# Performance work log

Hardware: AMD Instinct MI355X
Metric: run time of the kernel (lower is better)

Reference implementation:

```python
import jax, jax.numpy as jnp
from jax import lax
import numpy as np
import math

B, T, D, H, DFF, L = 64, 351, 512, 8, 1024, 3
DK = D // H
SQRT_DIM = math.sqrt(D)


def setup_inputs() -> dict:
    key = jax.random.key(0)
    ks = jax.random.split(key, 32)
    s = 0.02
    n = lambda k, shape, sc=s: jax.random.normal(k, shape, jnp.float32) * sc
    inp = {
        'x': jax.random.normal(ks[0], (B, T, D), jnp.float32),
        'mask': jax.random.normal(ks[1], (B, T, D), jnp.float32),  # float stream: used as pos_embedding inside attention
        'pos_emb': n(ks[2], (L, T, D)),           # Encoder.pos_embedding_{1,2,3}
        'Wq': n(ks[3], (L, D, D)), 'bq': jnp.zeros((L, D), jnp.float32),
        'Wk': n(ks[4], (L, D, D)), 'bk': jnp.zeros((L, D), jnp.float32),
        'Wv': n(ks[5], (L, D, D)), 'bv': jnp.zeros((L, D), jnp.float32),
        'Wp': n(ks[6], (L, D, D)),                 # pos_proj, no bias
        'u_bias': n(ks[7], (L, H, DK)), 'v_bias': n(ks[8], (L, H, DK)),
        'Wo': n(ks[9], (L, D, D)), 'bo': jnp.zeros((L, D), jnp.float32),
        'ln1_a': jnp.ones((L, D), jnp.float32), 'ln1_b': jnp.zeros((L, D), jnp.float32),
        'ln2_a': jnp.ones((L, D), jnp.float32), 'ln2_b': jnp.zeros((L, D), jnp.float32),
        'W1': n(ks[10], (L, DFF, D)), 'b1': jnp.zeros((L, DFF), jnp.float32),   # conv1d k=1
        'W2': n(ks[11], (L, D, DFF, 3)), 'b2': jnp.zeros((L, D), jnp.float32),  # conv1d k=3 pad=1
        'fn_a': jnp.ones((D,), jnp.float32), 'fn_b': jnp.zeros((D,), jnp.float32),
    }
    return inp


def layernorm(x, a, b, eps=1e-6):
    # torch: a*(x-mean)/(std+eps)+b with unbiased std (Bessel, n-1)
    mean = x.mean(-1, keepdims=True)
    xc = x - mean
    std = jnp.sqrt((xc * xc).sum(-1, keepdims=True) / (x.shape[-1] - 1))
    return a * xc / (std + eps) + b


def rel_shift(ps):
    # Transformer-XL relative shift via pad+reshape
    b, h, t1, t2 = ps.shape
    p = jnp.pad(ps, ((0, 0), (0, 0), (0, 0), (1, 0)))
    p = p.reshape(b, h, t2 + 1, t1)
    return p[:, :, 1:].reshape(b, h, t1, t2)


def attention(xn, pe, Wq, bq, Wk, bk, Wv, bv, Wp, u, v, Wo, bo):
    b, t, _ = xn.shape
    q = (xn @ Wq.T + bq).reshape(b, t, H, DK)
    k = (xn @ Wk.T + bk).reshape(b, t, H, DK)
    val = (xn @ Wv.T + bv).reshape(b, t, H, DK)
    p = (pe @ Wp.T).reshape(b, t, H, DK)
    content = jnp.einsum('bqhd,bkhd->bhqk', q + u, k)
    pos = rel_shift(jnp.einsum('bqhd,bkhd->bhqk', q + v, p))
    attn = jax.nn.softmax((content + pos) / SQRT_DIM, axis=-1)  # mask=None path; dropout inactive (eval)
    ctx = jnp.einsum('bhqk,bkhd->bqhd', attn, val).reshape(b, t, D)
    return ctx @ Wo.T + bo


def reference(x, mask, pos_emb, Wq, bq, Wk, bk, Wv, bv, Wp, u_bias, v_bias, Wo, bo,
              ln1_a, ln1_b, ln2_a, ln2_b, W1, b1, W2, b2, fn_a, fn_b):
    for i in range(L):
        x = x + pos_emb[i][None]
        # sublayer 0: pre-LN relative MHA with residual (stride_num[i]==1)
        xn = layernorm(x, ln1_a[i], ln1_b[i])
        x = x + attention(xn, mask, Wq[i], bq[i], Wk[i], bk[i], Wv[i], bv[i],
                          Wp[i], u_bias[i], v_bias[i], Wo[i], bo[i])
        # sublayer 1: pre-LN conv FFN (k=1 conv -> ReLU -> k=3 conv, pad 1, stride 1)
        xn = layernorm(x, ln2_a[i], ln2_b[i])
        h = jax.nn.relu(jnp.einsum('btd,fd->btf', xn, W1[i]) + b1[i])
        y = lax.conv_general_dilated(h.transpose(0, 2, 1), W2[i], (1,), [(1, 1)],
                                     dimension_numbers=('NCH', 'OIH', 'NCH'))
        x = x + (y + b2[i][None, :, None]).transpose(0, 2, 1)
    return layernorm(x, fn_a, fn_b)
```

## Files before the change

### kernel.cpp

```cpp
#include <hip/hip_runtime.h>
#include <hip/hip_bf16.h>

typedef __hip_bfloat16 bf16;
typedef __attribute__((ext_vector_type(8))) short short8;
typedef __attribute__((ext_vector_type(4))) float f32x4;

constexpr int BB  = 64;
constexpr int TT  = 351;
constexpr int DD  = 512;
constexpr int HH  = 8;
constexpr int DK  = 64;
constexpr int FF  = 1024;
constexpr int LL  = 3;
constexpr int MT  = BB * TT;
constexpr int TD  = TT * DD;

constexpr int QT  = 16;
constexpr int NQT = (TT + QT - 1) / QT;

constexpr size_t LW      = 3407872;
constexpr size_t OFF_QKV = 0;
constexpr size_t OFF_P   = 786432;
constexpr size_t OFF_O   = 1048576;
constexpr size_t OFF_W1  = 1310720;
constexpr size_t OFF_W2  = 1835008;

__device__ __forceinline__ float us2f(unsigned short u) {
    union { unsigned int i; float f; } c; c.i = ((unsigned int)u) << 16; return c.f;
}
__device__ __forceinline__ float bf2f(bf16 h) { return __bfloat162float(h); }
__device__ __forceinline__ bf16  f2bf(float f) { return __float2bfloat16(f); }
__device__ __forceinline__ float ldin(const void* p, size_t i, bool f32) {
    return f32 ? ((const float*)p)[i] : bf2f(((const bf16*)p)[i]);
}
__device__ __forceinline__ unsigned short f2us(float f) {
    bf16 h = f2bf(f); return *reinterpret_cast<unsigned short*>(&h);
}

__global__ void detect_kernel(const unsigned short* ln1a, int* flag) {
    if (threadIdx.x == 0 && blockIdx.x == 0)
        *flag = (ln1a[0] == 0) ? 1 : 0;
}

__global__ __launch_bounds__(256) void cvt_kernel(
    const void* __restrict__ src, size_t S, size_t slstride,
    bf16* __restrict__ dst, size_t doff, int nl, int mode,
    const int* __restrict__ dflag)
{
    const bool f32 = (*dflag != 0);
    size_t i = (size_t)blockIdx.x * 256 + threadIdx.x;
    size_t total = (size_t)nl * S;
    if (i >= total) return;
    size_t l = i / S, e = i - l * S;
    size_t se;
    if (mode == 1) {
        size_t j = e >> 19;
        size_t nf = e & ((1u << 19) - 1);
        size_t n = nf >> 10, f = nf & 1023;
        se = n * 3072 + f * 3 + j;
    } else se = e;
    dst[doff + l * LW + e] = f2bf(ldin(src, l * slstride + se, f32));
}

__global__ __launch_bounds__(256) void addpos_kernel(
    const void* __restrict__ xin, const void* __restrict__ pos, size_t posoff,
    float* __restrict__ xf, int init, const int* __restrict__ dflag)
{
    const bool f32 = (*dflag != 0);
    int i = blockIdx.x * 256 + threadIdx.x;
    if (i >= MT * DD) return;
    int td = i % TD;
    float p = ldin(pos, posoff + td, f32);
    if (init) xf[i] = ldin(xin, i, f32) + p;
    else      xf[i] += p;
}

__global__ __launch_bounds__(256) void ln_kernel(
    const float* __restrict__ xf, const void* __restrict__ ga, size_t gaoff,
    const void* __restrict__ gb, size_t gboff,
    void* __restrict__ out, int final_o, const int* __restrict__ dflag)
{
    const bool f32 = (*dflag != 0);
    __shared__ float red[256];
    const int row = blockIdx.x;
    const int tid = threadIdx.x;
    const float* xr = xf + (size_t)row * DD;
    float x0 = xr[tid], x1 = xr[tid + 256];

    red[tid] = x0 + x1;
    __syncthreads();
    for (int o = 128; o > 0; o >>= 1) {
        if (tid < o) red[tid] += red[tid + o];
        __syncthreads();
    }
    float mean = red[0] * (1.0f / 512.0f);
    __syncthreads();
    float c0 = x0 - mean, c1 = x1 - mean;
    red[tid] = c0 * c0 + c1 * c1;
    __syncthreads();
    for (int o = 128; o > 0; o >>= 1) {
        if (tid < o) red[tid] += red[tid + o];
        __syncthreads();
    }
    float stdv = sqrtf(red[0] * (1.0f / 511.0f));
    float inv = 1.0f / (stdv + 1e-6f);
    float v0 = ldin(ga, gaoff + tid,       f32) * c0 * inv + ldin(gb, gboff + tid,       f32);
    float v1 = ldin(ga, gaoff + tid + 256, f32) * c1 * inv + ldin(gb, gboff + tid + 256, f32);
    if (final_o && f32) {
        float* orow = (float*)out + (size_t)row * DD;
        orow[tid] = v0; orow[tid + 256] = v1;
    } else {
        bf16* orow = (bf16*)out + (size_t)row * DD;
        orow[tid] = f2bf(v0); orow[tid + 256] = f2bf(v1);
    }
}

__device__ __forceinline__ void xcd_remap(int& bx, int& by) {
    int gx = gridDim.x, gy = gridDim.y;
    int nb = gx * gy;
    int d  = by * gx + bx;
    if ((nb & 7) == 0) {
        int q = nb >> 3;
        d = (d & 7) * q + (d >> 3);
        bx = d % gx;
        by = d / gx;
    }
}

__global__ __launch_bounds__(256) void mgemm_kernel(
    const void* __restrict__ A, size_t aoff, int a_ext,
    const bf16* __restrict__ W,
    const void* __restrict__ b0, const void* __restrict__ b1p,
    const void* __restrict__ b2p, size_t boff,
    void* __restrict__ outp, int M, int N, int K, int mode, int chN,
    const int* __restrict__ dflag)
{
    const bool f32 = (*dflag != 0);
    const bool a32 = a_ext && f32;
    __shared__ unsigned short As[128][40];
    __shared__ unsigned short Bs[128][40];
    const int tid = threadIdx.x;
    int bx = blockIdx.x, by = blockIdx.y;
    xcd_remap(bx, by);
    const int n0 = bx * 128, m0 = by * 128;

    const int lane = tid & 63, wv = tid >> 6;
    const int wm = wv >> 1, wn = wv & 1;
    const int q = lane >> 4, lm = lane & 15;

    f32x4 acc[4][4] = {};

    for (int k0 = 0; k0 < K; k0 += 32) {
        #pragma unroll
        for (int part = 0; part < 2; ++part) {
            int idx = part * 256 + tid;
            int row = idx >> 2;
            int seg = (idx & 3) * 8;
            int grow = m0 + row; if (grow >= M) grow = M - 1;
            if (a32) {
                const float* ap = (const float*)A + aoff + (size_t)grow * K + k0 + seg;
                union { unsigned short us[8]; int4 v; } t;
                #pragma unroll
                for (int e = 0; e < 8; ++e) t.us[e] = f2us(ap[e]);
                *(int4*)&As[row][seg] = t.v;
            } else {
                *(int4*)&As[row][seg] =
                    *(const int4*)((const bf16*)A + aoff + (size_t)grow * K + k0 + seg);
            }
            *(int4*)&Bs[row][seg] =
                *(const int4*)(W + (size_t)(n0 + row) * K + k0 + seg);
        }
        __syncthreads();
        short8 af[4], bfv[4];
        #pragma unroll
        for (int i = 0; i < 4; ++i) af[i]  = *(const short8*)&As[wm * 64 + i * 16 + lm][q * 8];
        #pragma unroll
        for (int j = 0; j < 4; ++j) bfv[j] = *(const short8*)&Bs[wn * 64 + j * 16 + lm][q * 8];
        #pragma unroll
        for (int i = 0; i < 4; ++i)
            #pragma unroll
            for (int j = 0; j < 4; ++j)
                acc[i][j] = __builtin_amdgcn_mfma_f32_16x16x32_bf16(af[i], bfv[j], acc[i][j], 0, 0, 0);
        __syncthreads();
    }

    #pragma unroll
    for (int i = 0; i < 4; ++i) {
        #pragma unroll
        for (int j = 0; j < 4; ++j) {
            #pragma unroll
            for (int r = 0; r < 4; ++r) {
                int m = m0 + wm * 64 + i * 16 + q * 4 + r;
                if (m >= M) continue;
                int n = n0 + wn * 64 + j * 16 + lm;
                float c = acc[i][j][r];
                if (mode == 0) {
                    int which = n >> 9;
                    int nn = n & 511;
                    const void* bp = which == 0 ? b0 : (which == 1 ? b1p : b2p);
                    if (bp) c += ldin(bp, boff + nn, f32);
                    int b = m / TT, t = m - b * TT;
                    int h = nn >> 6, dk = nn & 63;
                    ((bf16*)outp)[(size_t)which * chN +
                                  ((((size_t)b * HH + h) * TT + t) * DK) + dk] = f2bf(c);
                } else if (mode == 1) {
                    if (b0) c += ldin(b0, boff + n, f32);
                    ((bf16*)outp)[(size_t)m * N + n] = f2bf(fmaxf(c, 0.0f));
                } else {
                    if (b0) c += ldin(b0, boff + n, f32);
                    ((float*)outp)[(size_t)m * DD + n] += c;
                }
            }
        }
    }
}

__global__ __launch_bounds__(256) void mconv_kernel(
    const bf16* __restrict__ Hb, const bf16* __restrict__ Wc,
    const void* __restrict__ bias, size_t boff,
    float* __restrict__ xf, int M, const int* __restrict__ dflag)
{
    const bool f32 = (*dflag != 0);
    __shared__ unsigned short As[128][40];
    __shared__ unsigned short Bs[128][40];
    const int tid = threadIdx.x;
    int bx = blockIdx.x, by = blockIdx.y;
    xcd_remap(bx, by);
    const int n0 = bx * 128, m0 = by * 128;

    const int lane = tid & 63, wv = tid >> 6;
    const int wm = wv >> 1, wn = wv & 1;
    const int q = lane >> 4, lm = lane & 15;

    int rowP[2], segP[2], mloadP[2], trowP[2];
    bool inrP[2];
    #pragma unroll
    for (int part = 0; part < 2; ++part) {
        int idx = part * 256 + tid;
        rowP[part] = idx >> 2;
        segP[part] = (idx & 3) * 8;
        int mrow = m0 + rowP[part];
        inrP[part] = mrow < M;
        int mload = inrP[part] ? mrow : (M - 1);
        mloadP[part] = mload;
        trowP[part] = mload % TT;
    }

    f32x4 acc[4][4] = {};

    for (int j = 0; j < 3; ++j) {
        for (int k0 = 0; k0 < FF; k0 += 32) {
            #pragma unroll
            for (int part = 0; part < 2; ++part) {
                int row = rowP[part], seg = segP[part];
                int ts = trowP[part] + j - 1;
                bool valid = inrP[part] && ts >= 0 && ts < TT;
                if (valid) {
                    *(int4*)&As[row][seg] =
                        *(const int4*)(Hb + (size_t)(mloadP[part] + j - 1) * FF + k0 + seg);
                } else {
                    int4 z = {0, 0, 0, 0};
                    *(int4*)&As[row][seg] = z;
                }
                *(int4*)&Bs[row][seg] =
                    *(const int4*)(Wc + (size_t)j * 524288 + (size_t)(n0 + row) * FF + k0 + seg);
            }
            __syncthreads();
            short8 af[4], bfv[4];
            #pragma unroll
            for (int i = 0; i < 4; ++i) af[i]  = *(const short8*)&As[wm * 64 + i * 16 + lm][q * 8];
            #pragma unroll
            for (int jj = 0; jj < 4; ++jj) bfv[jj] = *(const short8*)&Bs[wn * 64 + jj * 16 + lm][q * 8];
            #pragma unroll
            for (int i = 0; i < 4; ++i)
                #pragma unroll
                for (int jj = 0; jj < 4; ++jj)
                    acc[i][jj] = __builtin_amdgcn_mfma_f32_16x16x32_bf16(af[i], bfv[jj], acc[i][jj], 0, 0, 0);
            __syncthreads();
        }
    }

    #pragma unroll
    for (int i = 0; i < 4; ++i) {
        #pragma unroll
        for (int jj = 0; jj < 4; ++jj) {
            #pragma unroll
            for (int r = 0; r < 4; ++r) {
                int m = m0 + wm * 64 + i * 16 + q * 4 + r;
                if (m >= M) continue;
                int n = n0 + wn * 64 + jj * 16 + lm;
                xf[(size_t)m * DD + n] += acc[i][jj][r] + ldin(bias, boff + n, f32);
            }
        }
    }
}

__global__ __launch_bounds__(256, 4) void attn_kernel(
    const bf16* __restrict__ Q, const bf16* __restrict__ Kb,
    const bf16* __restrict__ V, const bf16* __restrict__ P,
    const void* __restrict__ ubias, const void* __restrict__ vbias, size_t uvoff,
    bf16* __restrict__ ctx, const int* __restrict__ dflag)
{
    const bool f32 = (*dflag != 0);
    const int d  = blockIdx.x + NQT * (blockIdx.y + HH * blockIdx.z);
    const int rr = d % (8 * NQT);
    const int g  = (d / (8 * NQT)) * 8 + (rr & 7);
    const int t  = rr >> 3;
    const int b  = g >> 3;
    const int h  = g & 7;
    const int q0 = t * QT;

    const int tid  = threadIdx.x;
    const int lane = tid & 63;
    const int wv   = tid >> 6;
    const int lm   = lane & 15;
    const int q8   = lane >> 4;

    __shared__ __align__(16) float S[QT][354];
    __shared__ __align__(16) unsigned short Abf[QT][356];
    __shared__ __align__(16) unsigned short qu[QT][72];
    __shared__ __align__(16) unsigned short qv[QT + 2][72];

    const size_t base = (((size_t)b * HH + h) * TT) * DK;
    const float scale = 0.04419417382415922f;

    for (int i = tid; i < (QT + 1) * 64; i += 256) {
        int q = i >> 6, dd = i & 63;
        int qrow = q0 + q;
        float qq = (qrow < TT) ? bf2f(Q[base + (size_t)qrow * DK + dd]) : 0.0f;
        float vb = ldin(vbias, uvoff + h * DK + dd, f32);
        qv[q][dd] = f2us((qq + vb) * scale);
        if (q < QT) {
            float ub = ldin(ubias, uvoff + h * DK + dd, f32);
            qu[q][dd] = f2us((qq + ub) * scale);
        }
    }
    __syncthreads();

    short8 kv0[6], kv1[6], pv0[6], pv1[6];
    #pragma unroll
    for (int it = 0; it < 6; ++it) {
        int jt = wv + it * 4;
        int kr = jt * 16 + lm; if (kr > TT - 1) kr = TT - 1;
        const short8* kp = (const short8*)(Kb + base + (size_t)kr * DK + q8 * 8);
        const short8* pp = (const short8*)(P  + base + (size_t)kr * DK + q8 * 8);
        kv0[it] = kp[0]; kv1[it] = kp[4];
        pv0[it] = pp[0]; pv1[it] = pp[4];
    }

    {
        short8 afa = *(const short8*)&qu[lm][q8 * 8];
        short8 afb = *(const short8*)&qu[lm][32 + q8 * 8];
        #pragma unroll
        for (int it = 0; it < 6; ++it) {
            int jt = wv + it * 4;
            if (jt >= NQT) break;
            f32x4 a0 = {};
            a0 = __builtin_amdgcn_mfma_f32_16x16x32_bf16(afa, kv0[it], a0, 0, 0, 0);
            a0 = __builtin_amdgcn_mfma_f32_16x16x32_bf16(afb, kv1[it], a0, 0, 0, 0);
            int col = jt * 16 + lm;
            #pragma unroll
            for (int r = 0; r < 4; ++r)
                S[q8 * 4 + r][col] = a0[r];
        }
    }
    __syncthreads();

    {
        short8 af0a = *(const short8*)&qv[lm][q8 * 8];
        short8 af0b = *(const short8*)&qv[lm][32 + q8 * 8];
        short8 af1a = {}, af1b = {};
        if (lm == 0) {
            af1a = *(const short8*)&qv[QT][q8 * 8];
            af1b = *(const short8*)&qv[QT][32 + q8 * 8];
        }
        #pragma unroll
        for (int it = 0; it < 6; ++it) {
            int jt = wv + it * 4;
            if (jt >= NQT) break;
            f32x4 ac0 = {}, ac1 = {};
            ac0 = __builtin_amdgcn_mfma_f32_16x16x32_bf16(af0a, pv0[it], ac0, 0, 0, 0);
            ac0 = __builtin_amdgcn_mfma_f32_16x16x32_bf16(af0b, pv1[it], ac0, 0, 0, 0);
            ac1 = __builtin_amdgcn_mfma_f32_16x16x32_bf16(af1a, pv0[it], ac1, 0, 0, 0);
            ac1 = __builtin_amdgcn_mfma_f32_16x16x32_bf16(af1b, pv1[it], ac1, 0, 0, 0);
            int j = jt * 16 + lm;
            if (j < TT) {
                #pragma unroll
                for (int i = 0; i < 2; ++i) {
                    #pragma unroll
                    for (int r = 0; r < 4; ++r) {
                        int rl = i * 16 + q8 * 4 + r;
                        int rg = q0 + rl;
                        float v = (i == 0) ? ac0[r] : ac1[r];
                        int cb  = (j + rg < TT - 1) ? 1 : 0;
                        int row = rl - cb;
                        int col = j + rg - (TT - 1) + cb * TT;
                        if (row >= 0 && row < QT) S[row][col] += v;
                    }
                }
            }
        }
    }
    __syncthreads();

    const unsigned short* vcol = (const unsigned short*)(V + base) + (wv * 16 + lm);
    short8 bvv[11];
    #pragma unroll
    for (int ks = 0; ks < 11; ++ks) {
        #pragma unroll
        for (int e = 0; e < 8; ++e) {
            int k = ks * 32 + q8 * 8 + e;
            bvv[ks][e] = (k < TT) ? (short)vcol[(size_t)k * DK] : (short)0;
        }
    }

    {
        const int row = tid >> 4, k0 = tid & 15;
        const float* Sr = S[row];
        float sv[22];
        #pragma unroll
        for (int i = 0; i < 22; ++i) {
            int k = k0 + 16 * i;
            sv[i] = (k < TT) ? Sr[k] : -1e30f;
        }
        float m = -1e30f;
        #pragma unroll
        for (int i = 0; i < 22; ++i) m = fmaxf(m, sv[i]);
        #pragma unroll
        for (int msk = 1; msk < 16; msk <<= 1) m = fmaxf(m, __shfl_xor(m, msk));
        float sum = 0.0f;
        #pragma unroll
        for (int i = 0; i < 22; ++i) {
            float e = __expf(sv[i] - m);
            sv[i] = e;
            sum += e;
        }
        #pragma unroll
        for (int msk = 1; msk < 16; msk <<= 1) sum += __shfl_xor(sum, msk);
        float rinv = 1.0f / sum;
        #pragma unroll
        for (int i = 0; i < 23; ++i) {
            int k = k0 + 16 * i;
            if (k < 356)
                Abf[row][k] = (k < TT && i < 22) ? f2us(sv[i] * rinv) : (unsigned short)0;
        }
    }
    __syncthreads();

    {
        f32x4 a0 = {};
        #pragma unroll
        for (int ks = 0; ks < 11; ++ks) {
            short8 av = *(const short8*)&Abf[lm][ks * 32 + q8 * 8];
            a0 = __builtin_amdgcn_mfma_f32_16x16x32_bf16(av, bvv[ks], a0, 0, 0, 0);
        }
        const int dd = wv * 16 + lm;
        #pragma unroll
        for (int r = 0; r < 4; ++r) {
            int qrow = q0 + q8 * 4 + r;
            if (qrow < TT)
                ctx[((size_t)b * TT + qrow) * DD + h * DK + dd] = f2bf(a0[r]);
        }
    }
}

extern "C" void kernel_launch(void* const* d_in, const int* in_sizes, int n_in,
                              void* d_out, int out_size, void* d_ws, size_t ws_size,
                              hipStream_t stream)
{
    (void)in_sizes; (void)n_in; (void)out_size;
    const void* x    = d_in[0];
    const void* mask = d_in[1];
    const void* pos  = d_in[2];
    const void* Wq   = d_in[3];
    const void* bq   = d_in[4];
    const void* Wk   = d_in[5];
    const void* bk   = d_in[6];
    const void* Wv   = d_in[7];
    const void* bv   = d_in[8];
    const void* Wp   = d_in[9];
    const void* ub   = d_in[10];
    const void* vbi  = d_in[11];
    const void* Wo   = d_in[12];
    const void* bo   = d_in[13];
    const void* l1a  = d_in[14];
    const void* l1b  = d_in[15];
    const void* l2a  = d_in[16];
    const void* l2b  = d_in[17];
    const void* W1   = d_in[18];
    const void* b1   = d_in[19];
    const void* W2   = d_in[20];
    const void* b2   = d_in[21];
    const void* fa   = d_in[22];
    const void* fb   = d_in[23];

    const size_t exf = (size_t)MT * DD;
    char* w = (char*)d_ws;
    int*   dflag = (int*)w;
    float* xf = (float*)(w + 256);
    bf16*  xn = (bf16*)(w + 256 + exf * 4);
    bf16*  sc = (bf16*)(w + 256 + exf * 6);
    bf16*  wbuf = (bf16*)d_out;

    const size_t fixed = 256 + exf * 6;
    int cha = 8;
    if      (ws_size >= fixed + (size_t)4 * 64 * TT * DD * 2) cha = 64;
    else if (ws_size >= fixed + (size_t)4 * 32 * TT * DD * 2) cha = 32;
    else if (ws_size >= fixed + (size_t)4 * 16 * TT * DD * 2) cha = 16;
    const int nca = BB / cha;
    const int ma  = cha * TT;
    const int chf = (cha * 2 > 64) ? 64 : cha * 2;
    const int ncf = BB / chf;
    const int mf  = chf * TT;
    const int chN = cha * TT * DD;

    bf16* qc = sc;
    bf16* pc = sc + (size_t)3 * chN;
    bf16* hb = sc;

    dim3 blk(256);
    dim3 g_ep((MT * DD + 255) / 256);
    dim3 g_ln(MT);
    dim3 g_qkv(12, (ma + 127) / 128);
    dim3 g_p(4, (ma + 127) / 128);
    dim3 g_attn(NQT, HH, cha);
    dim3 g_o(4, (MT + 127) / 128);
    dim3 g_f1(8, (mf + 127) / 128);
    dim3 g_cv(4, (mf + 127) / 128);

    detect_kernel<<<dim3(1), dim3(64), 0, stream>>>((const unsigned short*)l1a, dflag);

    auto cvt = [&](const void* src, size_t S, size_t doff, int mode) {
        dim3 g((unsigned)(((size_t)3 * S + 255) / 256));
        cvt_kernel<<<g, blk, 0, stream>>>(src, S, S, wbuf, doff, 3, mode, dflag);
    };
    cvt(Wq, 262144, OFF_QKV,          0);
    cvt(Wk, 262144, OFF_QKV + 262144, 0);
    cvt(Wv, 262144, OFF_QKV + 524288, 0);
    cvt(Wp, 262144, OFF_P,            0);
    cvt(Wo, 262144, OFF_O,            0);
    cvt(W1, 524288, OFF_W1,           0);
    cvt(W2, 1572864, OFF_W2,          1);

    for (int l = 0; l < LL; ++l) {
        const bf16* wl = wbuf + (size_t)l * LW;
        addpos_kernel<<<g_ep, blk, 0, stream>>>(x, pos, (size_t)l * TD, xf, l == 0, dflag);
        ln_kernel<<<g_ln, blk, 0, stream>>>(xf, l1a, (size_t)l * DD, l1b, (size_t)l * DD, xn, 0, dflag);
        for (int c = 0; c < nca; ++c) {
            bf16* xnc = xn + (size_t)c * ma * DD;
            mgemm_kernel<<<g_qkv, blk, 0, stream>>>(xnc, 0, 0, wl + OFF_QKV,
                bq, bk, bv, (size_t)l * DD, qc, ma, 1536, DD, 0, chN, dflag);
            mgemm_kernel<<<g_p, blk, 0, stream>>>(mask, (size_t)c * ma * DD, 1, wl + OFF_P,
                nullptr, nullptr, nullptr, 0, pc, ma, DD, DD, 0, 0, dflag);
            attn_kernel<<<g_attn, blk, 0, stream>>>(qc, qc + chN, qc + 2 * (size_t)chN, pc,
                ub, vbi, (size_t)l * HH * DK, xnc, dflag);
        }
        mgemm_kernel<<<g_o, blk, 0, stream>>>(xn, 0, 0, wl + OFF_O,
            bo, nullptr, nullptr, (size_t)l * DD, xf, MT, DD, DD, 2, 0, dflag);
        ln_kernel<<<g_ln, blk, 0, stream>>>(xf, l2a, (size_t)l * DD, l2b, (size_t)l * DD, xn, 0, dflag);
        for (int c = 0; c < ncf; ++c) {
            mgemm_kernel<<<g_f1, blk, 0, stream>>>(xn + (size_t)c * mf * DD, 0, 0, wl + OFF_W1,
                b1, nullptr, nullptr, (size_t)l * FF, hb, mf, FF, DD, 1, 0, dflag);
            mconv_kernel<<<g_cv, blk, 0, stream>>>(hb, wl + OFF_W2,
                b2, (size_t)l * DD, xf + (size_t)c * mf * DD, mf, dflag);
        }
    }
    ln_kernel<<<g_ln, blk, 0, stream>>>(xf, fa, 0, fb, 0, d_out, 1, dflag);
}
```

Before: 2.312 ms.

## Restructure attention: stage pos scores separately, transpose V through LDS with vector loads

The pos-score MFMA results are now written to a separate padded LDS buffer, and the rel-shift is applied as indexed reads during softmax. This replaces the scattered read-modify-write into S and removes one barrier. V is loaded with 16-byte vector loads, transposed through LDS that aliases S, and consumed in two halves, replacing strided 2-byte global gathers. LDS regions are reused between phases, which adds extra barriers and lowers occupancy launch bounds from 4 to 3.

```diff
diff --git a/kernel.cpp b/kernel.cpp
--- a/kernel.cpp
+++ b/kernel.cpp
@@ -17,6 +17,7 @@
 
 constexpr int QT  = 16;
 constexpr int NQT = (TT + QT - 1) / QT;
+constexpr int PSST = 362;
 
 constexpr size_t LW      = 3407872;
 constexpr size_t OFF_QKV = 0;
@@ -295,7 +296,7 @@
     }
 }
 
-__global__ __launch_bounds__(256, 4) void attn_kernel(
+__global__ __launch_bounds__(256, 3) void attn_kernel(
     const bf16* __restrict__ Q, const bf16* __restrict__ Kb,
     const bf16* __restrict__ V, const bf16* __restrict__ P,
     const void* __restrict__ ubias, const void* __restrict__ vbias, size_t uvoff,
@@ -316,14 +317,20 @@
     const int lm   = lane & 15;
     const int q8   = lane >> 4;
 
-    __shared__ __align__(16) float S[QT][354];
-    __shared__ __align__(16) unsigned short Abf[QT][356];
+    __shared__ __align__(16) char regA[22656];
+    __shared__ __align__(16) char regB[17 * PSST * 4];
     __shared__ __align__(16) unsigned short qu[QT][72];
-    __shared__ __align__(16) unsigned short qv[QT + 2][72];
+    __shared__ __align__(16) unsigned short qv[QT + 1][72];
+
+    float (*S)[354] = reinterpret_cast<float(*)[354]>(regA);
+    unsigned short (*Vt)[354] = reinterpret_cast<unsigned short(*)[354]>(regA);
+    float* PSf = reinterpret_cast<float*>(regB);
+    unsigned short (*Abf)[356] = reinterpret_cast<unsigned short(*)[356]>(regB);
 
     const size_t base = (((size_t)b * HH + h) * TT) * DK;
     const float scale = 0.04419417382415922f;
 
+    if (tid < 16) PSf[(tid + 1) * PSST] = 0.0f;
     for (int i = tid; i < (QT + 1) * 64; i += 256) {
         int q = i >> 6, dd = i & 63;
         int qrow = q0 + q;
@@ -364,7 +371,6 @@
                 S[q8 * 4 + r][col] = a0[r];
         }
     }
-    __syncthreads();
 
     {
         short8 af0a = *(const short8*)&qv[lm][q8 * 8];
@@ -385,43 +391,45 @@
             ac1 = __builtin_amdgcn_mfma_f32_16x16x32_bf16(af1b, pv1[it], ac1, 0, 0, 0);
             int j = jt * 16 + lm;
             if (j < TT) {
+                int fb = (q8 * 4) * PSST + 1 + j;
                 #pragma unroll
-                for (int i = 0; i < 2; ++i) {
-                    #pragma unroll
-                    for (int r = 0; r < 4; ++r) {
-                        int rl = i * 16 + q8 * 4 + r;
-                        int rg = q0 + rl;
-                        float v = (i == 0) ? ac0[r] : ac1[r];
-                        int cb  = (j + rg < TT - 1) ? 1 : 0;
-                        int row = rl - cb;
-                        int col = j + rg - (TT - 1) + cb * TT;
-                        if (row >= 0 && row < QT) S[row][col] += v;
-                    }
-                }
-            }
-        }
+                for (int r = 0; r < 4; ++r)
+                    PSf[fb + r * PSST] = ac0[r];
+                if (q8 == 0)
+                    PSf[16 * PSST + 1 + j] = ac1[0];
+            }
+        }
+    }
+
+    short8 vA[3][2], vB[3][2];
+    #pragma unroll
+    for (int it = 0; it < 3; ++it) {
+        int unit = it * 256 + tid; if (unit > 703) unit = 703;
+        int p2 = unit >> 2, dsg = unit & 3;
+        int k0r = p2 * 2;
+        int k1 = (k0r + 1 < TT) ? k0r + 1 : k0r;
+        const bf16* v0p = V + base + (size_t)k0r * DK;
+        const bf16* v1p = V + base + (size_t)k1 * DK;
+        vA[it][0] = *(const short8*)(v0p + dsg * 8);
+        vA[it][1] = *(const short8*)(v1p + dsg * 8);
+        vB[it][0] = *(const short8*)(v0p + 32 + dsg * 8);
+        vB[it][1] = *(const short8*)(v1p + 32 + dsg * 8);
     }
     __syncthreads();
 
-    const unsigned short* vcol = (const unsigned short*)(V + base) + (wv * 16 + lm);
-    short8 bvv[11];
-    #pragma unroll
-    for (int ks = 0; ks < 11; ++ks) {
-        #pragma unroll
-        for (int e = 0; e < 8; ++e) {
-            int k = ks * 32 + q8 * 8 + e;
-            bvv[ks][e] = (k < TT) ? (short)vcol[(size_t)k * DK] : (short)0;
-        }
-    }
-
+    const int row = tid >> 4, k0 = tid & 15;
+    float rinv, mval;
+    float sv[22];
     {
-        const int row = tid >> 4, k0 = tid & 15;
+        const int rgq = q0 + row;
         const float* Sr = S[row];
-        float sv[22];
+        const int baseA = row * PSST + 351 - rgq;
+        const int baseB = baseA + (PSST - 352);
         #pragma unroll
         for (int i = 0; i < 22; ++i) {
             int k = k0 + 16 * i;
-            sv[i] = (k < TT) ? Sr[k] : -1e30f;
+            float p = PSf[((k <= rgq) ? baseA : baseB) + k];
+            sv[i] = (k < TT) ? (Sr[k] + p) : -1e30f;
         }
         float m = -1e30f;
         #pragma unroll
@@ -437,30 +445,57 @@
         }
         #pragma unroll
         for (int msk = 1; msk < 16; msk <<= 1) sum += __shfl_xor(sum, msk);
-        float rinv = 1.0f / sum;
-        #pragma unroll
-        for (int i = 0; i < 23; ++i) {
-            int k = k0 + 16 * i;
-            if (k < 356)
-                Abf[row][k] = (k < TT && i < 22) ? f2us(sv[i] * rinv) : (unsigned short)0;
-        }
+        rinv = 1.0f / sum;
+        mval = m; (void)mval;
     }
     __syncthreads();
 
-    {
-        f32x4 a0 = {};
-        #pragma unroll
-        for (int ks = 0; ks < 11; ++ks) {
-            short8 av = *(const short8*)&Abf[lm][ks * 32 + q8 * 8];
-            a0 = __builtin_amdgcn_mfma_f32_16x16x32_bf16(av, bvv[ks], a0, 0, 0, 0);
-        }
-        const int dd = wv * 16 + lm;
-        #pragma unroll
-        for (int r = 0; r < 4; ++r) {
-            int qrow = q0 + q8 * 4 + r;
-            if (qrow < TT)
-                ctx[((size_t)b * TT + qrow) * DD + h * DK + dd] = f2bf(a0[r]);
-        }
+    #pragma unroll
+    for (int i = 0; i < 23; ++i) {
+        int k = k0 + 16 * i;
+        if (k < 356)
+            Abf[row][k] = (k < TT && i < 22) ? f2us(sv[i] * rinv) : (unsigned short)0;
+    }
+    __syncthreads();
+
+    #pragma unroll
+    for (int vh = 0; vh < 2; ++vh) {
+        #pragma unroll
+        for (int it = 0; it < 3; ++it) {
+            int unit = it * 256 + tid;
+            if (unit < 704) {
+                int p2 = unit >> 2, dsg = unit & 3;
+                int k0r = p2 * 2;
+                bool hasv1 = (k0r + 1 < TT);
+                const short8 v0 = vh ? vB[it][0] : vA[it][0];
+                const short8 v1 = vh ? vB[it][1] : vA[it][1];
+                #pragma unroll
+                for (int e = 0; e < 8; ++e) {
+                    unsigned int pk = (unsigned int)(unsigned short)v0[e];
+                    if (hasv1) pk |= ((unsigned int)(unsigned short)v1[e]) << 16;
+                    *(unsigned int*)&Vt[dsg * 8 + e][k0r] = pk;
+                }
+            }
+        }
+        __syncthreads();
+        if ((wv >> 1) == vh) {
+            f32x4 a0 = {};
+            const int ddl = (wv & 1) * 16 + lm;
+            #pragma unroll
+            for (int ks = 0; ks < 11; ++ks) {
+                short8 bv = *(const short8*)&Vt[ddl][ks * 32 + q8 * 8];
+                short8 av = *(const short8*)&Abf[lm][ks * 32 + q8 * 8];
+                a0 = __builtin_amdgcn_mfma_f32_16x16x32_bf16(av, bv, a0, 0, 0, 0);
+            }
+            const int dd = wv * 16 + lm;
+            #pragma unroll
+            for (int r = 0; r < 4; ++r) {
+                int qrow = q0 + q8 * 4 + r;
+                if (qrow < TT)
+                    ctx[((size_t)b * TT + qrow) * DD + h * DK + dd] = f2bf(a0[r]);
+            }
+        }
+        __syncthreads();
     }
 }
 
```

Result: slower. 2.490 ms (+7.7%).

## Store raw positional scores separately and apply rel-shift at softmax read

Applied to the files above, without the earlier changes.

The content and positional score passes no longer read-modify-write the same S buffer. Raw positional MFMA results go into their own padded shared buffer, and the relative shift is resolved by index arithmetic when the softmax loads its scores. This removes two barriers and the scattered conditional += into S. The softmax probabilities now reuse the positional buffer's shared memory, which needs an extra barrier, and launch bounds drop from 4 to 3 blocks per CU because the larger shared footprint lowers occupancy.

```diff
diff --git a/kernel.cpp b/kernel.cpp
--- a/kernel.cpp
+++ b/kernel.cpp
@@ -17,6 +17,7 @@
 
 constexpr int QT  = 16;
 constexpr int NQT = (TT + QT - 1) / QT;
+constexpr int PSST = 362;
 
 constexpr size_t LW      = 3407872;
 constexpr size_t OFF_QKV = 0;
@@ -295,7 +296,7 @@
     }
 }
 
-__global__ __launch_bounds__(256, 4) void attn_kernel(
+__global__ __launch_bounds__(256, 3) void attn_kernel(
     const bf16* __restrict__ Q, const bf16* __restrict__ Kb,
     const bf16* __restrict__ V, const bf16* __restrict__ P,
     const void* __restrict__ ubias, const void* __restrict__ vbias, size_t uvoff,
@@ -316,14 +317,19 @@
     const int lm   = lane & 15;
     const int q8   = lane >> 4;
 
-    __shared__ __align__(16) float S[QT][354];
-    __shared__ __align__(16) unsigned short Abf[QT][356];
+    __shared__ __align__(16) char regA[22656];
+    __shared__ __align__(16) char regB[17 * PSST * 4];
     __shared__ __align__(16) unsigned short qu[QT][72];
-    __shared__ __align__(16) unsigned short qv[QT + 2][72];
+    __shared__ __align__(16) unsigned short qv[QT + 1][72];
+
+    float (*S)[354] = reinterpret_cast<float(*)[354]>(regA);
+    float* PSf = reinterpret_cast<float*>(regB);
+    unsigned short (*Abf)[356] = reinterpret_cast<unsigned short(*)[356]>(regB);
 
     const size_t base = (((size_t)b * HH + h) * TT) * DK;
     const float scale = 0.04419417382415922f;
 
+    if (tid < 16) PSf[(tid + 1) * PSST] = 0.0f;
     for (int i = tid; i < (QT + 1) * 64; i += 256) {
         int q = i >> 6, dd = i & 63;
         int qrow = q0 + q;
@@ -364,7 +370,6 @@
                 S[q8 * 4 + r][col] = a0[r];
         }
     }
-    __syncthreads();
 
     {
         short8 af0a = *(const short8*)&qv[lm][q8 * 8];
@@ -385,23 +390,15 @@
             ac1 = __builtin_amdgcn_mfma_f32_16x16x32_bf16(af1b, pv1[it], ac1, 0, 0, 0);
             int j = jt * 16 + lm;
             if (j < TT) {
+                int fb = (q8 * 4) * PSST + 1 + j;
                 #pragma unroll
-                for (int i = 0; i < 2; ++i) {
-                    #pragma unroll
-                    for (int r = 0; r < 4; ++r) {
-                        int rl = i * 16 + q8 * 4 + r;
-                        int rg = q0 + rl;
-                        float v = (i == 0) ? ac0[r] : ac1[r];
-                        int cb  = (j + rg < TT - 1) ? 1 : 0;
-                        int row = rl - cb;
-                        int col = j + rg - (TT - 1) + cb * TT;
-                        if (row >= 0 && row < QT) S[row][col] += v;
-                    }
-                }
+                for (int r = 0; r < 4; ++r)
+                    PSf[fb + r * PSST] = ac0[r];
+                if (q8 == 0)
+                    PSf[16 * PSST + 1 + j] = ac1[0];
             }
         }
     }
-    __syncthreads();
 
     const unsigned short* vcol = (const unsigned short*)(V + base) + (wv * 16 + lm);
     short8 bvv[11];
@@ -413,15 +410,21 @@
             bvv[ks][e] = (k < TT) ? (short)vcol[(size_t)k * DK] : (short)0;
         }
     }
-
+    __syncthreads();
+
+    const int row = tid >> 4, k0 = tid & 15;
+    float rinv;
+    float sv[22];
     {
-        const int row = tid >> 4, k0 = tid & 15;
+        const int rgq = q0 + row;
         const float* Sr = S[row];
-        float sv[22];
+        const int baseA = row * PSST + 351 - rgq;
+        const int baseB = baseA + (PSST - 352);
         #pragma unroll
         for (int i = 0; i < 22; ++i) {
             int k = k0 + 16 * i;
-            sv[i] = (k < TT) ? Sr[k] : -1e30f;
+            float p = PSf[((k <= rgq) ? baseA : baseB) + k];
+            sv[i] = (k < TT) ? (Sr[k] + p) : -1e30f;
         }
         float m = -1e30f;
         #pragma unroll
@@ -437,13 +440,15 @@
         }
         #pragma unroll
         for (int msk = 1; msk < 16; msk <<= 1) sum += __shfl_xor(sum, msk);
-        float rinv = 1.0f / sum;
-        #pragma unroll
-        for (int i = 0; i < 23; ++i) {
-            int k = k0 + 16 * i;
-            if (k < 356)
-                Abf[row][k] = (k < TT && i < 22) ? f2us(sv[i] * rinv) : (unsigned short)0;
-        }
+        rinv = 1.0f / sum;
+    }
+    __syncthreads();
+
+    #pragma unroll
+    for (int i = 0; i < 23; ++i) {
+        int k = k0 + 16 * i;
+        if (k < 356)
+            Abf[row][k] = (k < TT && i < 22) ? f2us(sv[i] * rinv) : (unsigned short)0;
     }
     __syncthreads();
 
```

New measurement: 2.390 ms. 1.03x slower.
